# Kernel tuning notes

Hardware: AMD Instinct MI355X
Metric: run time of the kernel (lower is better)

The kernel has to match this reference:

```python
import jax, jax.numpy as jnp
import numpy as np

B, N, FEAT, HID, HEADS = 16, 1024, 512, 1024, 2

def setup_inputs() -> dict:
    key = jax.random.key(0)
    ks = jax.random.split(key, 20)
    s = 0.03
    d = {
        'Fs':  jax.random.normal(ks[0], (B, N, FEAT), jnp.float32),
        'Fq':  jax.random.normal(ks[1], (B, N, FEAT), jnp.float32),
        'Fms': jax.random.normal(ks[2], (B, N, FEAT), jnp.float32),
        'out_dim': N,
        'W1': jax.random.normal(ks[3], (FEAT, FEAT), jnp.float32) * s,
        'W2': jax.random.normal(ks[4], (FEAT, FEAT), jnp.float32) * s,
        'W3': jax.random.normal(ks[5], (FEAT, FEAT), jnp.float32) * s,
        'W4': jax.random.normal(ks[6], (FEAT, FEAT), jnp.float32) * s,
        'W5': jax.random.normal(ks[7], (FEAT, FEAT), jnp.float32) * s,
        'W6': jax.random.normal(ks[8], (FEAT, FEAT), jnp.float32) * s,
        'Wq': jax.random.normal(ks[9], (N, N), jnp.float32) * s,
        'Wk': jax.random.normal(ks[10], (N, N), jnp.float32) * s,
        'Wv': jax.random.normal(ks[11], (N, N), jnp.float32) * s,
        'ln_g': jnp.ones((N,), jnp.float32),
        'ln_b': jnp.zeros((N,), jnp.float32),
        'ffn_w1': jax.random.normal(ks[12], (N, HID), jnp.float32) * s,
        'ffn_w2': jax.random.normal(ks[13], (HID, N), jnp.float32) * s,
        'ffn_ln_g': jnp.ones((N,), jnp.float32),
        'ffn_ln_b': jnp.zeros((N,), jnp.float32),
    }
    return d

def _layernorm(x, g, b, eps):
    mu = x.mean(-1, keepdims=True)
    var = x.var(-1, keepdims=True)
    return (x - mu) * jax.lax.rsqrt(var + eps) * g + b

def _affinity(a, b, Wa, Wb, cl):
    # softmax((a Wa)(b Wb)^T / sqrt(cl)) over last axis
    s = jnp.einsum('bnc,bmc->bnm', a @ Wa, b @ Wb) / jnp.sqrt(jnp.float32(cl))
    return jax.nn.softmax(s, axis=-1)

def reference(Fs, Fq, Fms, out_dim, W1, W2, W3, W4, W5, W6, Wq, Wk, Wv,
              ln_g, ln_b, ffn_w1, ffn_w2, ffn_ln_g, ffn_ln_b):
    ass = _affinity(Fms, Fms, W1, W2, Fms.shape[2])   # [B,N,N]
    asq = _affinity(Fs, Fq, W3, W4, Fs.shape[2])      # [B,N,N]
    aqq = _affinity(Fq, Fq, W5, W6, Fq.shape[2])      # [B,N,N]

    Q, K, V = asq @ Wq, ass @ Wk, asq @ Wv            # [B,N,C], C=N
    Bb, Nn, C = Q.shape
    g = C // HEADS
    def heads(x):
        return x.reshape(Bb, Nn, HEADS, g).transpose(0, 2, 1, 3)  # [B,h,N,g]
    Qs, Ks, Vs = heads(Q), heads(K), heads(V)
    attn = jax.nn.softmax(jnp.einsum('bhqg,bhkg->bhqk', Qs, Ks) / jnp.sqrt(jnp.float32(g)), axis=-1)
    o = jnp.einsum('bhqk,bhkg->bhqg', attn, Vs)
    o = o.transpose(0, 2, 1, 3).reshape(Bb, Nn, C)

    x = _layernorm(o + aqq, ln_g, ln_b, 1e-5)
    y = jnp.maximum(x @ ffn_w1, 0.0) @ ffn_w2 + x     # dropout = identity (eval)
    y = _layernorm(y, ffn_ln_g, ffn_ln_b, 1e-6)
    return y
```

## Files before the change

### kernel.cpp

```cpp
#include <hip/hip_runtime.h>
#include <cstdint>

static constexpr long long Bb = 16, Nn = 1024, FE = 512;
static constexpr long long BN = Bb * Nn;
static constexpr long long E1e = BN * FE;
static constexpr long long E2n = BN * Nn;

static constexpr long long O_WT  = 0;
static constexpr long long SZ_W512 = FE * FE * 2;
static constexpr long long O_WQT = O_WT + 6 * SZ_W512;
static constexpr long long SZ_W1K = Nn * Nn * 2;
static constexpr long long O_WKT = O_WQT + SZ_W1K;
static constexpr long long O_WVT = O_WKT + SZ_W1K;
static constexpr long long O_F1T = O_WVT + SZ_W1K;
static constexpr long long O_F2T = O_F1T + SZ_W1K;
static constexpr long long O_SLOTS = O_F2T + SZ_W1K;
static constexpr long long SLOT = E2n * 2;
static constexpr long long O_S0 = O_SLOTS;
static constexpr long long O_S1 = O_S0 + SLOT;
static constexpr long long O_S2 = O_S1 + SLOT;
static constexpr long long O_E0 = O_S2 + SLOT;
static constexpr long long O_E1 = O_E0 + SLOT;
static constexpr long long O_E2 = O_E1 + SLOT;
static constexpr long long WS_NEED = O_E2 + SLOT;
static constexpr long long O_FMSB = O_E1;
static constexpr long long O_FSB  = O_E1 + E1e * 2;
static constexpr long long O_FQB  = O_E2;
static constexpr long long O_C2   = O_E2 + E1e * 2;

typedef __attribute__((ext_vector_type(8))) short short8;
typedef __attribute__((ext_vector_type(4))) float f32x4;

static __device__ __forceinline__ unsigned short f2bf(float f) {
  union { float f; unsigned u; } x; x.f = f;
  unsigned r = x.u + 0x7FFFu + ((x.u >> 16) & 1u);
  return (unsigned short)(r >> 16);
}
static __device__ __forceinline__ float bf2f(unsigned short h) {
  union { unsigned u; float f; } x; x.u = ((unsigned)h) << 16; return x.f;
}
static __device__ __forceinline__ void gload16(const void* g, void* l) {
  __builtin_amdgcn_global_load_lds(
      (const __attribute__((address_space(1))) unsigned int*)g,
      (__attribute__((address_space(3))) unsigned int*)l, 16, 0, 0);
}

template <int EP>
__global__ __launch_bounds__(512, 2) void gemm256(
    const unsigned short* __restrict__ A, long long sA, long long hA, int lda,
    const unsigned short* __restrict__ B, long long sB, long long hB, int ldb,
    void* __restrict__ Cv, long long sC, long long hC, int ldc,
    const void* __restrict__ Rv, long long sR, int K) {
  extern __shared__ unsigned short lds[];
  const int tid = threadIdx.x;
  const int lane = tid & 63;
  const int wave = tid >> 6;
  const int wm = wave >> 2, wn = wave & 3;
  const int lrow = lane & 15, quad = lane >> 4;

  const int gx = gridDim.x;
  const int nxy = gx * gridDim.y;
  const int nwg = nxy * gridDim.z;
  int wg = blockIdx.x + gx * blockIdx.y + nxy * blockIdx.z;
  wg = (wg & 7) * (nwg >> 3) + (wg >> 3);
  const int bz = wg / nxy;
  const int rem = wg - bz * nxy;
  const int by = rem / gx;
  const int bx = rem - by * gx;
  const int z1 = bz & 15, z2 = bz >> 4;

  const long long bm = (long long)bx * 256;
  const long long bn = (long long)by * 256;
  const unsigned short* Ab = A + z1 * sA + z2 * hA + bm * lda;
  const unsigned short* Bp = B + z1 * sB + z2 * hB + bn * ldb;

  const int srow = tid >> 2;
  const int scol = ((tid & 3) ^ ((tid >> 3) & 3)) * 8;
  unsigned short* ldst = lds + tid * 8;

  const int swq = (quad ^ ((lrow >> 1) & 3)) * 8;
  const int a_off = (wm * 128 + lrow) * 32 + swq;
  const int b_off = 8192 + (wn * 64 + lrow) * 32 + swq;

  f32x4 acc[8][4];
#pragma unroll
  for (int m = 0; m < 8; ++m)
#pragma unroll
    for (int n = 0; n < 4; ++n) acc[m][n] = (f32x4){0.f, 0.f, 0.f, 0.f};

  short8 af[8], bfr[4];
  auto READ_A0 = [&](int tt) {
    const unsigned short* lb = lds + (tt & 3) * 16384;
    bfr[0] = *(const short8*)&lb[b_off + 0 * 512];
    bfr[1] = *(const short8*)&lb[b_off + 1 * 512];
    bfr[2] = *(const short8*)&lb[b_off + 2 * 512];
    bfr[3] = *(const short8*)&lb[b_off + 3 * 512];
#pragma unroll
    for (int m = 0; m < 4; ++m) af[m] = *(const short8*)&lb[a_off + m * 512];
  };
  auto READ_A1 = [&](int tt) {
    const unsigned short* lb = lds + (tt & 3) * 16384;
#pragma unroll
    for (int m = 4; m < 8; ++m) af[m] = *(const short8*)&lb[a_off + m * 512];
  };
  auto MFMA_H = [&](int m0) {
    __builtin_amdgcn_s_setprio(1);
#pragma unroll
    for (int m = m0; m < m0 + 4; ++m)
#pragma unroll
      for (int n = 0; n < 4; ++n)
        acc[m][n] = __builtin_amdgcn_mfma_f32_16x16x32_bf16(af[m], bfr[n], acc[m][n], 0, 0, 0);
    __builtin_amdgcn_s_setprio(0);
  };
  auto STAGE = [&](int tt) {
    unsigned short* d = ldst + (tt & 3) * 16384;
    const long long ko = (long long)tt * 32 + scol;
    gload16(Ab + (long long)srow * lda + ko, d);
    gload16(Ab + (long long)(srow + 128) * lda + ko, d + 4096);
    gload16(Bp + (long long)srow * ldb + ko, d + 8192);
    gload16(Bp + (long long)(srow + 128) * ldb + ko, d + 12288);
  };

  const int nt = K >> 5;
  STAGE(0); STAGE(1); STAGE(2);
  asm volatile("s_waitcnt vmcnt(8)" ::: "memory");
  __builtin_amdgcn_s_barrier();
  int t = 0;
  for (; t < nt - 3; ++t) {
    unsigned short* d = ldst + ((t + 3) & 3) * 16384;
    const long long ko = (long long)(t + 3) * 32 + scol;
    READ_A0(t);
    gload16(Ab + (long long)srow * lda + ko, d);
    gload16(Ab + (long long)(srow + 128) * lda + ko, d + 4096);
    __builtin_amdgcn_s_barrier();
    MFMA_H(0);
    __builtin_amdgcn_s_barrier();
    READ_A1(t);
    gload16(Bp + (long long)srow * ldb + ko, d + 8192);
    gload16(Bp + (long long)(srow + 128) * ldb + ko, d + 12288);
    asm volatile("s_waitcnt vmcnt(8)" ::: "memory");
    __builtin_amdgcn_s_barrier();
    MFMA_H(4);
    __builtin_amdgcn_s_barrier();
  }
  READ_A0(t);
  __builtin_amdgcn_s_barrier();
  MFMA_H(0);
  __builtin_amdgcn_s_barrier();
  READ_A1(t);
  asm volatile("s_waitcnt vmcnt(4)" ::: "memory");
  __builtin_amdgcn_s_barrier();
  MFMA_H(4);
  __builtin_amdgcn_s_barrier();
  ++t;
  READ_A0(t);
  __builtin_amdgcn_s_barrier();
  MFMA_H(0);
  __builtin_amdgcn_s_barrier();
  READ_A1(t);
  asm volatile("s_waitcnt vmcnt(0)" ::: "memory");
  __builtin_amdgcn_s_barrier();
  MFMA_H(4);
  __builtin_amdgcn_s_barrier();
  ++t;
  READ_A0(t);
  MFMA_H(0);
  READ_A1(t);
  MFMA_H(4);

  const long long cm = bm + wm * 128, cn = bn + wn * 64;
  const long long cz = z1 * sC + z2 * hC;
#pragma unroll
  for (int mt = 0; mt < 8; ++mt) {
#pragma unroll
    for (int ntl = 0; ntl < 4; ++ntl) {
      long long col = cn + ntl * 16 + lrow;
      long long row0 = cm + mt * 16 + quad * 4;
#pragma unroll
      for (int r = 0; r < 4; ++r) {
        long long row = row0 + r;
        float v = acc[mt][ntl][r];
        long long idx = cz + row * ldc + col;
        if (EP == 1) ((unsigned short*)Cv)[idx] = f2bf(v);
        else if (EP == 2) ((unsigned short*)Cv)[idx] = f2bf(v > 0.f ? v : 0.f);
        else {
          float rr = bf2f(((const unsigned short*)Rv)[z1 * sR + row * ldc + col]);
          ((float*)Cv)[idx] = v + rr;
        }
      }
    }
  }
}

__global__ __launch_bounds__(256) void cast3_k(const float* __restrict__ i0,
                                               const float* __restrict__ i1,
                                               const float* __restrict__ i2,
                                               unsigned short* o0, unsigned short* o1,
                                               unsigned short* o2) {
  const float* in = (blockIdx.y == 0) ? i0 : (blockIdx.y == 1) ? i1 : i2;
  unsigned short* out = (blockIdx.y == 0) ? o0 : (blockIdx.y == 1) ? o1 : o2;
  long long i = (long long)blockIdx.x * 256 + threadIdx.x;
  float4 v = ((const float4*)in)[i];
  ushort4 o; o.x = f2bf(v.x); o.y = f2bf(v.y); o.z = f2bf(v.z); o.w = f2bf(v.w);
  ((ushort4*)out)[i] = o;
}

__global__ __launch_bounds__(256) void tcast6_k(const float* p0, const float* p1,
                                                const float* p2, const float* p3,
                                                const float* p4, const float* p5,
                                                unsigned short* outb, int rows, int cols) {
  const float* src[6] = {p0, p1, p2, p3, p4, p5};
  const float* in = src[blockIdx.z];
  unsigned short* out = outb + (long long)blockIdx.z * rows * cols;
  __shared__ float t[32][33];
  const int c0 = blockIdx.x * 32, r0 = blockIdx.y * 32;
  const int tx = threadIdx.x, ty = threadIdx.y;
#pragma unroll
  for (int i = 0; i < 4; ++i) {
    int r = r0 + ty + i * 8;
    t[ty + i * 8][tx] = in[(long long)r * cols + c0 + tx];
  }
  __syncthreads();
#pragma unroll
  for (int i = 0; i < 4; ++i) {
    int c = c0 + ty + i * 8;
    out[(long long)c * rows + r0 + tx] = f2bf(t[tx][ty + i * 8]);
  }
}

__global__ __launch_bounds__(256) void softmax_bf(unsigned short* __restrict__ S, float scale) {
  __shared__ float redA[4], redB[4];
  const long long row = blockIdx.x;
  const int t = threadIdx.x, wave = t >> 6, lane = t & 63;
  ushort4 u = ((ushort4*)(S + row * 1024))[t];
  float v0 = bf2f(u.x) * scale, v1 = bf2f(u.y) * scale, v2 = bf2f(u.z) * scale, v3 = bf2f(u.w) * scale;
  float m = fmaxf(fmaxf(v0, v1), fmaxf(v2, v3));
#pragma unroll
  for (int o = 32; o; o >>= 1) m = fmaxf(m, __shfl_down(m, o));
  if (lane == 0) redA[wave] = m;
  __syncthreads();
  m = fmaxf(fmaxf(redA[0], redA[1]), fmaxf(redA[2], redA[3]));
  float e0 = __expf(v0 - m), e1 = __expf(v1 - m), e2 = __expf(v2 - m), e3 = __expf(v3 - m);
  float s = e0 + e1 + e2 + e3;
#pragma unroll
  for (int o = 32; o; o >>= 1) s += __shfl_down(s, o);
  if (lane == 0) redB[wave] = s;
  __syncthreads();
  s = redB[0] + redB[1] + redB[2] + redB[3];
  float inv = 1.f / s;
  ushort4 ob; ob.x = f2bf(e0 * inv); ob.y = f2bf(e1 * inv); ob.z = f2bf(e2 * inv); ob.w = f2bf(e3 * inv);
  ((ushort4*)(S + row * 1024))[t] = ob;
}

__global__ __launch_bounds__(256) void ln1_k(const unsigned short* __restrict__ O,
                                             const unsigned short* __restrict__ Aq,
                                             const float* __restrict__ g, const float* __restrict__ b,
                                             unsigned short* __restrict__ xb) {
  __shared__ float redA[4], redB[4];
  const long long row = blockIdx.x;
  const int t = threadIdx.x, wave = t >> 6, lane = t & 63;
  ushort4 ou = ((const ushort4*)(O + row * 1024))[t];
  ushort4 au = ((const ushort4*)(Aq + row * 1024))[t];
  float v0 = bf2f(ou.x) + bf2f(au.x), v1 = bf2f(ou.y) + bf2f(au.y);
  float v2 = bf2f(ou.z) + bf2f(au.z), v3 = bf2f(ou.w) + bf2f(au.w);
  float s = v0 + v1 + v2 + v3;
  float q = v0 * v0 + v1 * v1 + v2 * v2 + v3 * v3;
#pragma unroll
  for (int o = 32; o; o >>= 1) { s += __shfl_down(s, o); q += __shfl_down(q, o); }
  if (lane == 0) { redA[wave] = s; redB[wave] = q; }
  __syncthreads();
  float S = redA[0] + redA[1] + redA[2] + redA[3];
  float Q = redB[0] + redB[1] + redB[2] + redB[3];
  float mu = S * (1.f / 1024.f);
  float var = Q * (1.f / 1024.f) - mu * mu;
  float rs = rsqrtf(var + 1e-5f);
  float4 gg = ((const float4*)g)[t], bbv = ((const float4*)b)[t];
  ushort4 ob;
  ob.x = f2bf((v0 - mu) * rs * gg.x + bbv.x);
  ob.y = f2bf((v1 - mu) * rs * gg.y + bbv.y);
  ob.z = f2bf((v2 - mu) * rs * gg.z + bbv.z);
  ob.w = f2bf((v3 - mu) * rs * gg.w + bbv.w);
  ((ushort4*)(xb + row * 1024))[t] = ob;
}

__global__ __launch_bounds__(256) void ln2_k(const float* __restrict__ Y,
                                             const float* __restrict__ g, const float* __restrict__ b,
                                             float* __restrict__ out, float eps) {
  __shared__ float redA[4], redB[4];
  const long long row = blockIdx.x;
  const int t = threadIdx.x, wave = t >> 6, lane = t & 63;
  float4 v = ((const float4*)(Y + row * 1024))[t];
  float s = v.x + v.y + v.z + v.w;
  float q = v.x * v.x + v.y * v.y + v.z * v.z + v.w * v.w;
#pragma unroll
  for (int o = 32; o; o >>= 1) { s += __shfl_down(s, o); q += __shfl_down(q, o); }
  if (lane == 0) { redA[wave] = s; redB[wave] = q; }
  __syncthreads();
  float S = redA[0] + redA[1] + redA[2] + redA[3];
  float Q = redB[0] + redB[1] + redB[2] + redB[3];
  float mu = S * (1.f / 1024.f);
  float var = Q * (1.f / 1024.f) - mu * mu;
  float rs = rsqrtf(var + eps);
  float4 gg = ((const float4*)g)[t], bbv = ((const float4*)b)[t];
  float4 o;
  o.x = (v.x - mu) * rs * gg.x + bbv.x;
  o.y = (v.y - mu) * rs * gg.y + bbv.y;
  o.z = (v.z - mu) * rs * gg.z + bbv.z;
  o.w = (v.w - mu) * rs * gg.w + bbv.w;
  ((float4*)(out + row * 1024))[t] = o;
}

extern "C" void kernel_launch(void* const* d_in, const int* in_sizes, int n_in,
                              void* d_out, int out_size, void* d_ws, size_t ws_size,
                              hipStream_t stream) {
  (void)in_sizes; (void)n_in; (void)out_size;
  if (ws_size < (size_t)WS_NEED) return;

  static int attr_once = []() {
    (void)hipFuncSetAttribute(reinterpret_cast<const void*>(&gemm256<1>),
                              hipFuncAttributeMaxDynamicSharedMemorySize, 131072);
    (void)hipFuncSetAttribute(reinterpret_cast<const void*>(&gemm256<2>),
                              hipFuncAttributeMaxDynamicSharedMemorySize, 131072);
    (void)hipFuncSetAttribute(reinterpret_cast<const void*>(&gemm256<3>),
                              hipFuncAttributeMaxDynamicSharedMemorySize, 131072);
    return 0;
  }();
  (void)attr_once;

  const float* Fs  = (const float*)d_in[0];
  const float* Fq  = (const float*)d_in[1];
  const float* Fms = (const float*)d_in[2];
  const float* Wm[6] = {(const float*)d_in[4], (const float*)d_in[5], (const float*)d_in[6],
                        (const float*)d_in[7], (const float*)d_in[8], (const float*)d_in[9]};
  const float* Wq = (const float*)d_in[10];
  const float* Wk = (const float*)d_in[11];
  const float* Wv = (const float*)d_in[12];
  const float* ln_g = (const float*)d_in[13];
  const float* ln_b = (const float*)d_in[14];
  const float* fw1 = (const float*)d_in[15];
  const float* fw2 = (const float*)d_in[16];
  const float* fg = (const float*)d_in[17];
  const float* fb = (const float*)d_in[18];
  float* out = (float*)d_out;
  uint8_t* ws = (uint8_t*)d_ws;
  auto U16 = [&](long long off) { return (unsigned short*)(ws + off); };

  const float inv_sqrt512 = 0.04419417382415922f;
  dim3 blk(256);

  auto gemm = [&](int ep, const unsigned short* A, long long sA, long long hA, int lda,
                  const unsigned short* B, long long sB, long long hB, int ldb,
                  void* C, long long sC, long long hC, int ldc, const void* R, long long sR,
                  int M, int N, int K, int batch) {
    dim3 g(M / 256, N / 256, batch);
    dim3 b(512);
    switch (ep) {
      case 1: gemm256<1><<<g, b, 131072, stream>>>(A, sA, hA, lda, B, sB, hB, ldb, C, sC, hC, ldc, R, sR, K); break;
      case 2: gemm256<2><<<g, b, 131072, stream>>>(A, sA, hA, lda, B, sB, hB, ldb, C, sC, hC, ldc, R, sR, K); break;
      default: gemm256<3><<<g, b, 131072, stream>>>(A, sA, hA, lda, B, sB, hB, ldb, C, sC, hC, ldc, R, sR, K); break;
    }
  };

  tcast6_k<<<dim3(16, 16, 6), dim3(32, 8), 0, stream>>>(
      Wm[0], Wm[1], Wm[2], Wm[3], Wm[4], Wm[5], U16(O_WT), 512, 512);
  tcast6_k<<<dim3(32, 32, 5), dim3(32, 8), 0, stream>>>(
      Wq, Wk, Wv, fw1, fw2, fw2 , U16(O_WQT), 1024, 1024);
  cast3_k<<<dim3(E1e / 4 / 256, 3), blk, 0, stream>>>(
      Fs, Fq, Fms, U16(O_FSB), U16(O_FQB), U16(O_FMSB));

  gemm(1, U16(O_FMSB), 16777216, 0, 512, U16(O_WT), 786432, 0, 512,
       U16(O_S0), 16777216, 0, 1024, nullptr, 0, (int)BN, 1024, 512, 2);
  gemm(1, U16(O_S0), Nn * 1024, 0, 1024, U16(O_S0) + 512, Nn * 1024, 0, 1024,
       U16(O_E0), Nn * Nn, 0, 1024, nullptr, 0, 1024, 1024, 512, (int)Bb);
  gemm(1, U16(O_FSB), 8388608, 0, 512, U16(O_WT + 2 * SZ_W512), 786432, 0, 512,
       U16(O_C2), -58720256LL, 0, 512, nullptr, 0, (int)BN, 512, 512, 2);
  gemm(1, U16(O_C2), Nn * 512, 0, 512, U16(O_S1), Nn * 1024, 0, 1024,
       U16(O_E1), Nn * Nn, 0, 1024, nullptr, 0, 1024, 1024, 512, (int)Bb);
  gemm(1, U16(O_S1) + 512, Nn * 1024, 0, 1024, U16(O_S2), Nn * 512, 0, 512,
       U16(O_E2), Nn * Nn, 0, 1024, nullptr, 0, 1024, 1024, 512, (int)Bb);
  softmax_bf<<<dim3(3 * BN), blk, 0, stream>>>(U16(O_E0), inv_sqrt512);

  const unsigned short* assB = U16(O_E0);

  gemm(1, assB, Nn * Nn, E2n, 1024,
       U16(O_WKT), 0, -(long long)(SZ_W1K / 2), 1024,
       U16(O_S1), Nn * 1024, -(long long)E2n, 1024,
       nullptr, 0, 1024, 1024, 1024, 32);
  gemm(1, U16(O_WVT), 0, 0, 1024, U16(O_E1), Nn * Nn, 0, 1024, U16(O_S2), Nn * Nn, 0, 1024,
       nullptr, 0, 1024, 1024, 1024, (int)Bb);

  gemm(1, U16(O_S0), Nn * 1024, 512, 1024, U16(O_S1), Nn * 1024, 512, 1024,
       U16(O_E0), Nn * Nn, 16 * Nn * Nn, 1024, nullptr, 0, 1024, 1024, 512, 32);
  softmax_bf<<<dim3(2 * BN), blk, 0, stream>>>(U16(O_E0), inv_sqrt512);

  gemm(1, U16(O_E0), Nn * Nn, 16 * Nn * Nn, 1024, U16(O_S2), Nn * Nn, 512 * 1024, 1024,
       U16(O_S0), Nn * 1024, 512, 1024, nullptr, 0, 1024, 512, 1024, 32);

  ln1_k<<<dim3(BN), blk, 0, stream>>>(U16(O_S0), U16(O_E2), ln_g, ln_b, U16(O_S1));

  gemm(2, U16(O_S1), 0, 0, 1024, U16(O_F1T), 0, 0, 1024, U16(O_S2), 0, 0, 1024,
       nullptr, 0, (int)BN, 1024, 1024, 1);

  gemm(3, U16(O_S2), 0, 0, 1024, U16(O_F2T), 0, 0, 1024, out, 0, 0, 1024,
       U16(O_S1), 0, (int)BN, 1024, 1024, 1);

  ln2_k<<<dim3(BN), blk, 0, stream>>>(out, fg, fb, out, 1e-6f);
}
```

Measured before the change: 718.5 us.

## Fold projection weight pairs into one matrix per affinity and remap XCD scheduling

Each affinity score (a Wa)(b Wb)^T is rewritten as a (Wa Wb^T) b^T. A small batched GEMM first builds the three 512x512 products Wa·Wb^T. Only one BN×512 projection per affinity is then computed, replacing the two projections previously needed, and the scores are formed against the raw bf16 features. The workspace layout and softmax launches are reshuffled to match. The workgroup-to-XCD remap now also handles counts not divisible by 8. Rounding the fused weight product to bf16 changes numerics slightly.

```diff
diff --git a/kernel.cpp b/kernel.cpp
--- a/kernel.cpp
+++ b/kernel.cpp
@@ -23,10 +23,8 @@
 static constexpr long long O_E1 = O_E0 + SLOT;
 static constexpr long long O_E2 = O_E1 + SLOT;
 static constexpr long long WS_NEED = O_E2 + SLOT;
-static constexpr long long O_FMSB = O_E1;
-static constexpr long long O_FSB  = O_E1 + E1e * 2;
-static constexpr long long O_FQB  = O_E2;
-static constexpr long long O_C2   = O_E2 + E1e * 2;
+static constexpr long long O_FB = O_E0;
+static constexpr long long O_GT = O_S2;
 
 typedef __attribute__((ext_vector_type(8))) short short8;
 typedef __attribute__((ext_vector_type(4))) float f32x4;
@@ -62,7 +60,11 @@
   const int nxy = gx * gridDim.y;
   const int nwg = nxy * gridDim.z;
   int wg = blockIdx.x + gx * blockIdx.y + nxy * blockIdx.z;
-  wg = (wg & 7) * (nwg >> 3) + (wg >> 3);
+  {
+    const int q = nwg >> 3, r = nwg & 7;
+    const int xcd = wg & 7, blk = wg >> 3;
+    wg = (xcd < r ? xcd * (q + 1) : r * (q + 1) + (xcd - r) * q) + blk;
+  }
   const int bz = wg / nxy;
   const int rem = wg - bz * nxy;
   const int by = rem / gx;
@@ -361,42 +363,43 @@
     }
   };
 
-  tcast6_k<<<dim3(16, 16, 6), dim3(32, 8), 0, stream>>>(
-      Wm[0], Wm[1], Wm[2], Wm[3], Wm[4], Wm[5], U16(O_WT), 512, 512);
+  unsigned short* Wc = U16(O_WT);
+  cast3_k<<<dim3(256, 3), blk, 0, stream>>>(Wm[0], Wm[1], Wm[2], Wc, Wc + 262144, Wc + 2 * 262144);
+  cast3_k<<<dim3(256, 3), blk, 0, stream>>>(Wm[3], Wm[4], Wm[5], Wc + 3 * 262144, Wc + 4 * 262144, Wc + 5 * 262144);
   tcast6_k<<<dim3(32, 32, 5), dim3(32, 8), 0, stream>>>(
       Wq, Wk, Wv, fw1, fw2, fw2 , U16(O_WQT), 1024, 1024);
+  unsigned short* FB = U16(O_FB);
   cast3_k<<<dim3(E1e / 4 / 256, 3), blk, 0, stream>>>(
-      Fs, Fq, Fms, U16(O_FSB), U16(O_FQB), U16(O_FMSB));
-
-  gemm(1, U16(O_FMSB), 16777216, 0, 512, U16(O_WT), 786432, 0, 512,
-       U16(O_S0), 16777216, 0, 1024, nullptr, 0, (int)BN, 1024, 512, 2);
-  gemm(1, U16(O_S0), Nn * 1024, 0, 1024, U16(O_S0) + 512, Nn * 1024, 0, 1024,
-       U16(O_E0), Nn * Nn, 0, 1024, nullptr, 0, 1024, 1024, 512, (int)Bb);
-  gemm(1, U16(O_FSB), 8388608, 0, 512, U16(O_WT + 2 * SZ_W512), 786432, 0, 512,
-       U16(O_C2), -58720256LL, 0, 512, nullptr, 0, (int)BN, 512, 512, 2);
-  gemm(1, U16(O_C2), Nn * 512, 0, 512, U16(O_S1), Nn * 1024, 0, 1024,
-       U16(O_E1), Nn * Nn, 0, 1024, nullptr, 0, 1024, 1024, 512, (int)Bb);
-  gemm(1, U16(O_S1) + 512, Nn * 1024, 0, 1024, U16(O_S2), Nn * 512, 0, 512,
+      Fms, Fs, Fq, FB, FB + E1e, FB + 2 * E1e);
+
+  gemm(1, Wc + 262144, 524288, 0, 512, Wc, 524288, 0, 512,
+       U16(O_GT), 262144, 0, 512, nullptr, 0, 512, 512, 512, 3);
+  gemm(1, FB, E1e, 0, 512, U16(O_GT), 262144, 0, 512,
+       U16(O_S0), E1e, 0, 512, nullptr, 0, (int)BN, 512, 512, 3);
+  gemm(1, U16(O_S0), Nn * 512, 0, 512, FB, Nn * 512, 0, 512,
        U16(O_E2), Nn * Nn, 0, 1024, nullptr, 0, 1024, 1024, 512, (int)Bb);
-  softmax_bf<<<dim3(3 * BN), blk, 0, stream>>>(U16(O_E0), inv_sqrt512);
-
-  const unsigned short* assB = U16(O_E0);
-
-  gemm(1, assB, Nn * Nn, E2n, 1024,
+  gemm(1, U16(O_S0) + E1e, Nn * 512, E1e, 512, FB + 2 * E1e, Nn * 512, 0, 512,
+       U16(O_E0), Nn * Nn, -(long long)E2n, 1024, nullptr, 0, 1024, 1024, 512, 32);
+  softmax_bf<<<dim3(2 * BN), blk, 0, stream>>>(U16(O_S2), inv_sqrt512);
+  softmax_bf<<<dim3(BN), blk, 0, stream>>>(U16(O_E2), inv_sqrt512);
+
+  gemm(1, U16(O_E2), Nn * Nn, -(long long)(2 * E2n), 1024,
        U16(O_WKT), 0, -(long long)(SZ_W1K / 2), 1024,
        U16(O_S1), Nn * 1024, -(long long)E2n, 1024,
        nullptr, 0, 1024, 1024, 1024, 32);
-  gemm(1, U16(O_WVT), 0, 0, 1024, U16(O_E1), Nn * Nn, 0, 1024, U16(O_S2), Nn * Nn, 0, 1024,
+  gemm(1, U16(O_WVT), 0, 0, 1024, U16(O_E0), Nn * Nn, 0, 1024, U16(O_E1), Nn * Nn, 0, 1024,
        nullptr, 0, 1024, 1024, 1024, (int)Bb);
 
   gemm(1, U16(O_S0), Nn * 1024, 512, 1024, U16(O_S1), Nn * 1024, 512, 1024,
-       U16(O_E0), Nn * Nn, 16 * Nn * Nn, 1024, nullptr, 0, 1024, 1024, 512, 32);
-  softmax_bf<<<dim3(2 * BN), blk, 0, stream>>>(U16(O_E0), inv_sqrt512);
-
-  gemm(1, U16(O_E0), Nn * Nn, 16 * Nn * Nn, 1024, U16(O_S2), Nn * Nn, 512 * 1024, 1024,
+       U16(O_E2), Nn * Nn, -(long long)(2 * E2n), 1024, nullptr, 0, 1024, 1024, 512, 32);
+  softmax_bf<<<dim3(BN), blk, 0, stream>>>(U16(O_E2), inv_sqrt512);
+  softmax_bf<<<dim3(BN), blk, 0, stream>>>(U16(O_E0), inv_sqrt512);
+
+  gemm(1, U16(O_E2), Nn * Nn, -(long long)(2 * E2n), 1024,
+       U16(O_E1), Nn * Nn, (long long)(512 * 1024), 1024,
        U16(O_S0), Nn * 1024, 512, 1024, nullptr, 0, 1024, 512, 1024, 32);
 
-  ln1_k<<<dim3(BN), blk, 0, stream>>>(U16(O_S0), U16(O_E2), ln_g, ln_b, U16(O_S1));
+  ln1_k<<<dim3(BN), blk, 0, stream>>>(U16(O_S0), U16(O_S2), ln_g, ln_b, U16(O_S1));
 
   gemm(2, U16(O_S1), 0, 0, 1024, U16(O_F1T), 0, 0, 1024, U16(O_S2), 0, 0, 1024,
        nullptr, 0, (int)BN, 1024, 1024, 1);
```

New measurement: 702.5 us. -2.2%, faster.
